# Optimization experiments

Measured on AMD Instinct MI355X. Metric: run time of the kernel, lower is better.

Reference implementation:

```python
import jax, jax.numpy as jnp
import numpy as np

N_SENT = 20  # sentence_number


def setup_inputs() -> dict:
    key = jax.random.key(0)
    k1, k2, k3, k4, k5 = jax.random.split(key, 5)
    B, S, D, U = 2048, 800, 100, 50
    inputs = jax.random.normal(k1, (B, S + 1, D), dtype=jnp.float32)
    # keras 'random_normal' initializer default stddev = 0.05
    vw = 0.05 * jax.random.normal(k2, (U, 1), dtype=jnp.float32)
    wh = 0.05 * jax.random.normal(k3, (U, D), dtype=jnp.float32)
    wu = 0.05 * jax.random.normal(k4, (U, D), dtype=jnp.float32)
    bw = 0.05 * jax.random.normal(k5, (U, 1), dtype=jnp.float32)
    return {"inputs": inputs, "vw": vw, "wh": wh, "wu": wu, "bw": bw}


def reference(inputs, vw, wh, wu, bw):
    # inputs: [B, S+1, D]; last row of each item is the user vector
    sent = inputs[:, :-1, :]          # [B, S, D]
    uvec = inputs[:, -1, :]           # [B, D]
    B, S, D = sent.shape
    sec = S // N_SENT
    h = sent.reshape(B, N_SENT, sec, D)               # sections of sentences
    # wu @ user_vec + bw  -> per-batch additive bias  [B, units]
    wub = uvec @ wu.T + bw[:, 0]
    # tanh(h @ wh.T + wub)                              [B, n, s, units]
    t = jnp.tanh(jnp.einsum('bnsd,ud->bnsu', h, wh) + wub[:, None, None, :])
    e = jnp.einsum('bnsu,u->bns', t, vw[:, 0])          # attention logits
    alpha = jax.nn.softmax(e, axis=-1)                  # softmax over section
    out = jnp.einsum('bns,bnsd->bnd', alpha, h)         # weighted pooling
    return out  # [B, N_SENT, D]
```

## Files before the change

kernel.cpp:

```cpp
#include <hip/hip_runtime.h>
#include <hip/hip_bf16.h>
#include <stdint.h>

#define NB    2048
#define NSENT 20
#define SEC   40
#define DD    100
#define UU    50
#define SP1   801

typedef __attribute__((ext_vector_type(8))) short bf16x8;
typedef __attribute__((ext_vector_type(4))) float f32x4;

__device__ __forceinline__ unsigned short f2bf(float f) {
  unsigned u = __float_as_uint(f);
  unsigned r = u + 0x7fffu + ((u >> 16) & 1u);
  return (unsigned short)(r >> 16);
}

__global__ __launch_bounds__(64, 2) void doc_kernel(
    const float* __restrict__ inputs, const float* __restrict__ vw,
    const float* __restrict__ wh, const float* __restrict__ wu,
    const float* __restrict__ bw, float* __restrict__ out) {
  __shared__ __align__(16) unsigned short hs[48 * 136];
  __shared__ float alpha[SEC];
  const int lane = threadIdx.x;
  const int b = blockIdx.x;
  const int col = lane & 15, grp = lane >> 4;

  const float4* base4 = (const float4*)(inputs + (size_t)b * SP1 * DD);

  float4 stage[16];
  #pragma unroll
  for (int j = 0; j < 15; ++j) stage[j] = base4[j * 64 + lane];
  if (lane < 40) stage[15] = base4[960 + lane];

  for (int i = lane; i < 360; i += 64) {
    int row = i / 9, c = i - row * 9;
    uint2 z; z.x = 0u; z.y = 0u;
    *(uint2*)&hs[row * 136 + 100 + c * 4] = z;
  }

  bf16x8 bfrag[4][4];
  #pragma unroll
  for (int nt = 0; nt < 4; ++nt) {
    int u = nt * 16 + col;
    #pragma unroll
    for (int kt = 0; kt < 4; ++kt) {
      bf16x8 f;
      #pragma unroll
      for (int j = 0; j < 8; ++j) {
        int k = kt * 32 + grp * 8 + j;
        float v = (u < UU && k < DD) ? wh[u * DD + k] : 0.f;
        f[j] = (short)f2bf(v);
      }
      bfrag[nt][kt] = f;
    }
  }

  float wubacc;
  {
    int ur = lane < UU ? lane : UU - 1;
    const float4* uv4 = (const float4*)(inputs + ((size_t)b * SP1 + SP1 - 1) * DD);
    const float4* wr4 = (const float4*)(wu + ur * DD);
    float a0 = bw[ur];
    #pragma unroll 5
    for (int q = 0; q < 25; ++q) {
      float4 uq = uv4[q], wq = wr4[q];
      a0 = fmaf(uq.x, wq.x, a0); a0 = fmaf(uq.y, wq.y, a0);
      a0 = fmaf(uq.z, wq.z, a0); a0 = fmaf(uq.w, wq.w, a0);
    }
    wubacc = a0;
  }
  float vwv[4], wubv[4];
  #pragma unroll
  for (int nt = 0; nt < 4; ++nt) {
    int u = nt * 16 + col;
    float wv = __shfl(wubacc, nt * 16 + col);
    vwv[nt] = (u < UU) ? vw[u] : 0.f;
    wubv[nt] = (u < UU) ? wv : 0.f;
  }

  float* outb = out + (size_t)b * NSENT * DD;

  #pragma unroll 1
  for (int t = 0; t < NSENT; ++t) {
    #pragma unroll
    for (int j = 0; j < 16; ++j) {
      if (j < 15 || lane < 40) {
        int idx = j * 64 + lane;
        int row = idx / 25, c4 = idx - row * 25;
        uint2 w;
        w.x = (unsigned)f2bf(stage[j].x) | ((unsigned)f2bf(stage[j].y) << 16);
        w.y = (unsigned)f2bf(stage[j].z) | ((unsigned)f2bf(stage[j].w) << 16);
        *(uint2*)&hs[row * 136 + c4 * 4] = w;
      }
    }

    if (t + 1 < NSENT) {
      const float4* nb4 = base4 + (size_t)(t + 1) * 1000;
      #pragma unroll
      for (int j = 0; j < 15; ++j) stage[j] = nb4[j * 64 + lane];
      if (lane < 40) stage[15] = nb4[960 + lane];
    }

    f32x4 acc[3][4];
    #pragma unroll
    for (int mt = 0; mt < 3; ++mt)
      #pragma unroll
      for (int nt = 0; nt < 4; ++nt) {
        f32x4 z = {0.f, 0.f, 0.f, 0.f};
        acc[mt][nt] = z;
      }
    #pragma unroll
    for (int kt = 0; kt < 4; ++kt) {
      #pragma unroll
      for (int mt = 0; mt < 3; ++mt) {
        bf16x8 af = *(const bf16x8*)&hs[(mt * 16 + col) * 136 + kt * 32 + grp * 8];
        #pragma unroll
        for (int nt = 0; nt < 4; ++nt)
          acc[mt][nt] = __builtin_amdgcn_mfma_f32_16x16x32_bf16(af, bfrag[nt][kt], acc[mt][nt], 0, 0, 0);
      }
    }

    float el[3][4];
    #pragma unroll
    for (int mt = 0; mt < 3; ++mt) {
      #pragma unroll
      for (int r = 0; r < 4; ++r) {
        float s = 0.f;
        #pragma unroll
        for (int nt = 0; nt < 4; ++nt) {
          float x = acc[mt][nt][r] + wubv[nt];
          x = fminf(fmaxf(x, -15.f), 15.f);
          float E = __expf(2.f * x);
          float tt = 1.f - 2.f / (E + 1.f);
          s = fmaf(tt, vwv[nt], s);
        }
        s += __shfl_xor(s, 1);
        s += __shfl_xor(s, 2);
        s += __shfl_xor(s, 4);
        s += __shfl_xor(s, 8);
        el[mt][r] = s;
      }
    }

    float mx = -1e30f;
    #pragma unroll
    for (int mt = 0; mt < 3; ++mt)
      #pragma unroll
      for (int r = 0; r < 4; ++r) {
        int row = mt * 16 + grp * 4 + r;
        if (row < SEC) mx = fmaxf(mx, el[mt][r]);
      }
    mx = fmaxf(mx, __shfl_xor(mx, 16));
    mx = fmaxf(mx, __shfl_xor(mx, 32));
    float p[3][4];
    float sum = 0.f;
    #pragma unroll
    for (int mt = 0; mt < 3; ++mt)
      #pragma unroll
      for (int r = 0; r < 4; ++r) {
        int row = mt * 16 + grp * 4 + r;
        float pe = (row < SEC) ? __expf(el[mt][r] - mx) : 0.f;
        p[mt][r] = pe;
        sum += pe;
      }
    sum += __shfl_xor(sum, 16);
    sum += __shfl_xor(sum, 32);
    float rinv = 1.f / sum;
    if (col == 0) {
      #pragma unroll
      for (int mt = 0; mt < 3; ++mt)
        #pragma unroll
        for (int r = 0; r < 4; ++r) {
          int row = mt * 16 + grp * 4 + r;
          if (row < SEC) alpha[row] = p[mt][r] * rinv;
        }
    }

    if (lane < DD / 2) {
      float f0 = 0.f, f1 = 0.f;
      #pragma unroll 8
      for (int s = 0; s < SEC; ++s) {
        float a = alpha[s];
        unsigned w = *(const unsigned*)&hs[s * 136 + lane * 2];
        f0 = fmaf(a, __uint_as_float(w << 16), f0);
        f1 = fmaf(a, __uint_as_float(w & 0xffff0000u), f1);
      }
      float2 o; o.x = f0; o.y = f1;
      *(float2*)(outb + t * DD + lane * 2) = o;
    }
  }
}

extern "C" void kernel_launch(void* const* d_in, const int* in_sizes, int n_in,
                              void* d_out, int out_size, void* d_ws, size_t ws_size,
                              hipStream_t stream) {
  const float* inputs = (const float*)d_in[0];
  const float* vw     = (const float*)d_in[1];
  const float* wh     = (const float*)d_in[2];
  const float* wu     = (const float*)d_in[3];
  const float* bw     = (const float*)d_in[4];
  float* out = (float*)d_out;

  doc_kernel<<<NB, 64, 0, stream>>>(inputs, vw, wh, wu, bw, out);
}
```

Before: 177.2 us.

## Split per-batch work across four waves with double-buffered LDS tile

The block grows from one wave to four. Each wave computes one 16-unit slice of the projection using MFMA, with wh as the A operand. The per-section logits and the pooled outputs are reduced across waves through shared memory. The hs buffer is double-buffered, and rcp intrinsics replace the divisions. The change is meant to cut per-thread register staging and raise memory-level parallelism. In exchange it adds several block-wide barriers per section.

```diff
diff --git a/kernel.cpp b/kernel.cpp
--- a/kernel.cpp
+++ b/kernel.cpp
@@ -8,43 +8,50 @@
 #define DD    100
 #define UU    50
 #define SP1   801
+#define STRIDE 136
 
 typedef __attribute__((ext_vector_type(8))) short bf16x8;
 typedef __attribute__((ext_vector_type(4))) float f32x4;
 
-__device__ __forceinline__ unsigned short f2bf(float f) {
+__device__ __forceinline__ unsigned f2bf(float f) {
   unsigned u = __float_as_uint(f);
   unsigned r = u + 0x7fffu + ((u >> 16) & 1u);
-  return (unsigned short)(r >> 16);
+  return r >> 16;
 }
 
-__global__ __launch_bounds__(64, 2) void doc_kernel(
+__global__ __launch_bounds__(256, 4) void doc_kernel(
     const float* __restrict__ inputs, const float* __restrict__ vw,
     const float* __restrict__ wh, const float* __restrict__ wu,
     const float* __restrict__ bw, float* __restrict__ out) {
-  __shared__ __align__(16) unsigned short hs[48 * 136];
-  __shared__ float alpha[SEC];
-  const int lane = threadIdx.x;
-  const int b = blockIdx.x;
-  const int col = lane & 15, grp = lane >> 4;
+  __shared__ __align__(16) unsigned short hs[2][48 * STRIDE];
+  __shared__ __align__(16) float epart[3 * 16 * 4];
+  __shared__ float alphas[SEC];
+  __shared__ __align__(16) float2 opart[50 * 4];
+
+  const int tid  = threadIdx.x;
+  const int w    = tid >> 6, lane = tid & 63;
+  const int col  = lane & 15, grp = lane >> 4;
+  const int b    = blockIdx.x;
 
   const float4* base4 = (const float4*)(inputs + (size_t)b * SP1 * DD);
 
-  float4 stage[16];
+  float4 stage[4];
   #pragma unroll
-  for (int j = 0; j < 15; ++j) stage[j] = base4[j * 64 + lane];
-  if (lane < 40) stage[15] = base4[960 + lane];
-
-  for (int i = lane; i < 360; i += 64) {
-    int row = i / 9, c = i - row * 9;
-    uint2 z; z.x = 0u; z.y = 0u;
-    *(uint2*)&hs[row * 136 + 100 + c * 4] = z;
-  }
-
-  bf16x8 bfrag[4][4];
-  #pragma unroll
-  for (int nt = 0; nt < 4; ++nt) {
-    int u = nt * 16 + col;
+  for (int j = 0; j < 4; ++j) {
+    int idx = j * 256 + tid;
+    if (idx < 1000) stage[j] = base4[idx];
+  }
+
+  {
+    uint4 z; z.x = z.y = z.z = z.w = 0u;
+    uint4* p = (uint4*)&hs[0][0];
+    #pragma unroll 1
+    for (int i = tid; i < 2 * 48 * STRIDE / 8; i += 256) p[i] = z;
+  }
+
+  bf16x8 afrag[4];
+  {
+    int u = w * 16 + col;
     #pragma unroll
     for (int kt = 0; kt < 4; ++kt) {
       bf16x8 f;
@@ -54,7 +61,7 @@
         float v = (u < UU && k < DD) ? wh[u * DD + k] : 0.f;
         f[j] = (short)f2bf(v);
       }
-      bfrag[nt][kt] = f;
+      afrag[kt] = f;
     }
   }
 
@@ -72,125 +79,127 @@
     }
     wubacc = a0;
   }
-  float vwv[4], wubv[4];
+  float vwr[4], wubr[4];
   #pragma unroll
-  for (int nt = 0; nt < 4; ++nt) {
-    int u = nt * 16 + col;
-    float wv = __shfl(wubacc, nt * 16 + col);
-    vwv[nt] = (u < UU) ? vw[u] : 0.f;
-    wubv[nt] = (u < UU) ? wv : 0.f;
-  }
+  for (int r = 0; r < 4; ++r) {
+    int u = w * 16 + grp * 4 + r;
+    float wv = __shfl(wubacc, u & 63);
+    bool val = (u < UU);
+    vwr[r]  = val ? vw[u] : 0.f;
+    wubr[r] = val ? wv : 0.f;
+  }
+
+  __syncthreads();
 
   float* outb = out + (size_t)b * NSENT * DD;
+  int cur = 0;
 
   #pragma unroll 1
   for (int t = 0; t < NSENT; ++t) {
     #pragma unroll
-    for (int j = 0; j < 16; ++j) {
-      if (j < 15 || lane < 40) {
-        int idx = j * 64 + lane;
+    for (int j = 0; j < 4; ++j) {
+      int idx = j * 256 + tid;
+      if (idx < 1000) {
         int row = idx / 25, c4 = idx - row * 25;
-        uint2 w;
-        w.x = (unsigned)f2bf(stage[j].x) | ((unsigned)f2bf(stage[j].y) << 16);
-        w.y = (unsigned)f2bf(stage[j].z) | ((unsigned)f2bf(stage[j].w) << 16);
-        *(uint2*)&hs[row * 136 + c4 * 4] = w;
-      }
-    }
+        uint2 wv;
+        wv.x = f2bf(stage[j].x) | (f2bf(stage[j].y) << 16);
+        wv.y = f2bf(stage[j].z) | (f2bf(stage[j].w) << 16);
+        *(uint2*)&hs[cur][row * STRIDE + c4 * 4] = wv;
+      }
+    }
+    __syncthreads();
 
     if (t + 1 < NSENT) {
       const float4* nb4 = base4 + (size_t)(t + 1) * 1000;
       #pragma unroll
-      for (int j = 0; j < 15; ++j) stage[j] = nb4[j * 64 + lane];
-      if (lane < 40) stage[15] = nb4[960 + lane];
-    }
-
-    f32x4 acc[3][4];
-    #pragma unroll
-    for (int mt = 0; mt < 3; ++mt)
-      #pragma unroll
-      for (int nt = 0; nt < 4; ++nt) {
-        f32x4 z = {0.f, 0.f, 0.f, 0.f};
-        acc[mt][nt] = z;
-      }
+      for (int j = 0; j < 4; ++j) {
+        int idx = j * 256 + tid;
+        if (idx < 1000) stage[j] = nb4[idx];
+      }
+    }
+    __builtin_amdgcn_sched_barrier(0);
+
+    f32x4 acc[3];
+    #pragma unroll
+    for (int st = 0; st < 3; ++st) { f32x4 z = {0.f,0.f,0.f,0.f}; acc[st] = z; }
     #pragma unroll
     for (int kt = 0; kt < 4; ++kt) {
       #pragma unroll
-      for (int mt = 0; mt < 3; ++mt) {
-        bf16x8 af = *(const bf16x8*)&hs[(mt * 16 + col) * 136 + kt * 32 + grp * 8];
-        #pragma unroll
-        for (int nt = 0; nt < 4; ++nt)
-          acc[mt][nt] = __builtin_amdgcn_mfma_f32_16x16x32_bf16(af, bfrag[nt][kt], acc[mt][nt], 0, 0, 0);
-      }
-    }
-
-    float el[3][4];
-    #pragma unroll
-    for (int mt = 0; mt < 3; ++mt) {
+      for (int st = 0; st < 3; ++st) {
+        bf16x8 hf = *(const bf16x8*)&hs[cur][(st * 16 + col) * STRIDE + kt * 32 + grp * 8];
+        acc[st] = __builtin_amdgcn_mfma_f32_16x16x32_bf16(afrag[kt], hf, acc[st], 0, 0, 0);
+      }
+    }
+
+    #pragma unroll
+    for (int st = 0; st < 3; ++st) {
+      float s = 0.f;
       #pragma unroll
       for (int r = 0; r < 4; ++r) {
-        float s = 0.f;
-        #pragma unroll
-        for (int nt = 0; nt < 4; ++nt) {
-          float x = acc[mt][nt][r] + wubv[nt];
-          x = fminf(fmaxf(x, -15.f), 15.f);
-          float E = __expf(2.f * x);
-          float tt = 1.f - 2.f / (E + 1.f);
-          s = fmaf(tt, vwv[nt], s);
-        }
-        s += __shfl_xor(s, 1);
-        s += __shfl_xor(s, 2);
-        s += __shfl_xor(s, 4);
-        s += __shfl_xor(s, 8);
-        el[mt][r] = s;
-      }
-    }
-
-    float mx = -1e30f;
-    #pragma unroll
-    for (int mt = 0; mt < 3; ++mt)
-      #pragma unroll
-      for (int r = 0; r < 4; ++r) {
-        int row = mt * 16 + grp * 4 + r;
-        if (row < SEC) mx = fmaxf(mx, el[mt][r]);
-      }
-    mx = fmaxf(mx, __shfl_xor(mx, 16));
-    mx = fmaxf(mx, __shfl_xor(mx, 32));
-    float p[3][4];
-    float sum = 0.f;
-    #pragma unroll
-    for (int mt = 0; mt < 3; ++mt)
-      #pragma unroll
-      for (int r = 0; r < 4; ++r) {
-        int row = mt * 16 + grp * 4 + r;
-        float pe = (row < SEC) ? __expf(el[mt][r] - mx) : 0.f;
-        p[mt][r] = pe;
-        sum += pe;
-      }
-    sum += __shfl_xor(sum, 16);
-    sum += __shfl_xor(sum, 32);
-    float rinv = 1.f / sum;
-    if (col == 0) {
-      #pragma unroll
-      for (int mt = 0; mt < 3; ++mt)
-        #pragma unroll
-        for (int r = 0; r < 4; ++r) {
-          int row = mt * 16 + grp * 4 + r;
-          if (row < SEC) alpha[row] = p[mt][r] * rinv;
-        }
-    }
-
-    if (lane < DD / 2) {
+        float x = acc[st][r] + wubr[r];
+        x = fminf(fmaxf(x, -15.f), 15.f);
+        float E = __expf(2.f * x);
+        float tt = 1.f - 2.f * __builtin_amdgcn_rcpf(E + 1.f);
+        s = fmaf(tt, vwr[r], s);
+      }
+      s += __shfl_xor(s, 16);
+      s += __shfl_xor(s, 32);
+      if (grp == 0) epart[st * 64 + col * 4 + w] = s;
+    }
+    __syncthreads();
+
+    f32x4 q0 = *(const f32x4*)&epart[0 * 64 + col * 4];
+    f32x4 q1 = *(const f32x4*)&epart[1 * 64 + col * 4];
+    f32x4 q2 = *(const f32x4*)&epart[2 * 64 + col * 4];
+    float e0 = (q0[0] + q0[1]) + (q0[2] + q0[3]);
+    float e1 = (q1[0] + q1[1]) + (q1[2] + q1[3]);
+    float e2 = (q2[0] + q2[1]) + (q2[2] + q2[3]);
+    float mx = fmaxf(e0, e1);
+    if (col < 8) mx = fmaxf(mx, e2);
+    mx = fmaxf(mx, __shfl_xor(mx, 1));
+    mx = fmaxf(mx, __shfl_xor(mx, 2));
+    mx = fmaxf(mx, __shfl_xor(mx, 4));
+    mx = fmaxf(mx, __shfl_xor(mx, 8));
+    float p0 = __expf(e0 - mx);
+    float p1 = __expf(e1 - mx);
+    float p2 = (col < 8) ? __expf(e2 - mx) : 0.f;
+    float sum = p0 + p1 + p2;
+    sum += __shfl_xor(sum, 1);
+    sum += __shfl_xor(sum, 2);
+    sum += __shfl_xor(sum, 4);
+    sum += __shfl_xor(sum, 8);
+    float rinv = __builtin_amdgcn_rcpf(sum);
+    if (w == 0 && grp == 0) {
+      alphas[col]      = p0 * rinv;
+      alphas[16 + col] = p1 * rinv;
+      if (col < 8) alphas[32 + col] = p2 * rinv;
+    }
+    __syncthreads();
+
+    if (lane < 50) {
       float f0 = 0.f, f1 = 0.f;
-      #pragma unroll 8
-      for (int s = 0; s < SEC; ++s) {
-        float a = alpha[s];
-        unsigned w = *(const unsigned*)&hs[s * 136 + lane * 2];
-        f0 = fmaf(a, __uint_as_float(w << 16), f0);
-        f1 = fmaf(a, __uint_as_float(w & 0xffff0000u), f1);
+      #pragma unroll
+      for (int i = 0; i < 10; ++i) {
+        int s = w * 10 + i;
+        float a = alphas[s];
+        unsigned hh = *(const unsigned*)&hs[cur][s * STRIDE + lane * 2];
+        f0 = fmaf(a, __uint_as_float(hh << 16), f0);
+        f1 = fmaf(a, __uint_as_float(hh & 0xffff0000u), f1);
       }
       float2 o; o.x = f0; o.y = f1;
+      opart[lane * 4 + w] = o;
+    }
+    __syncthreads();
+
+    if (w == 0 && lane < 50) {
+      f32x4 a0 = *(const f32x4*)&opart[lane * 4];
+      f32x4 a1 = *(const f32x4*)&opart[lane * 4 + 2];
+      float2 o;
+      o.x = (a0[0] + a0[2]) + (a1[0] + a1[2]);
+      o.y = (a0[1] + a0[3]) + (a1[1] + a1[3]);
       *(float2*)(outb + t * DD + lane * 2) = o;
     }
+    cur ^= 1;
   }
 }
 
@@ -204,5 +213,5 @@
   const float* bw     = (const float*)d_in[4];
   float* out = (float*)d_out;
 
-  doc_kernel<<<NB, 64, 0, stream>>>(inputs, vw, wh, wu, bw, out);
+  doc_kernel<<<NB, 256, 0, stream>>>(inputs, vw, wh, wu, bw, out);
 }
```

Result: faster. 165.4 us (-6.7%).
